# Performance work log

Hardware: AMD Instinct MI355X
Metric: run time of the kernel (lower is better)

Reference implementation:

```python
import jax, jax.numpy as jnp
import numpy as np

N_NODES = 200000
N_EDGES = 4000000  # doubled (w2b + b2w), matches edge_weight param size
N_W2B = 2000000


def gcn_conv(x, W, b, src, dst, ew, n):
    # PyG GCNConv with add_self_loops=True, symmetric normalization.
    loop = jnp.arange(n)
    src_sl = jnp.concatenate([src, loop])
    dst_sl = jnp.concatenate([dst, loop])
    w_sl = jnp.concatenate([ew, jnp.ones((n,), ew.dtype)])  # self-loop weight 1
    deg = jax.ops.segment_sum(w_sl, dst_sl, num_segments=n)
    dinv = jnp.where(deg > 0, jax.lax.rsqrt(deg), 0.0)
    norm = dinv[src_sl] * w_sl * dinv[dst_sl]          # [E+N]
    xw = x @ W                                          # [N, out]
    msg = xw[src_sl] * norm[:, None]                    # [E+N, out]
    out = jax.ops.segment_sum(msg, dst_sl, num_segments=n)
    return out + b


def setup_inputs() -> dict:
    key = jax.random.key(0)
    ks = jax.random.split(key, 16)
    h1, h2, h3, h4, out = 8, 16, 32, 4, 3
    inp = 7

    def lin_init(k, fan_in, fan_out):
        bound = 1.0 / np.sqrt(fan_in)
        kw, kb = jax.random.split(k)
        W = jax.random.uniform(kw, (fan_in, fan_out), jnp.float32, -bound, bound)
        b = jax.random.uniform(kb, (fan_out,), jnp.float32, -bound, bound)
        return W, b

    x = jax.random.normal(ks[0], (N_NODES, inp), jnp.float32)
    edge_index = jax.random.randint(ks[1], (2, N_EDGES), 0, N_NODES, jnp.int64)
    w2b = jax.random.randint(ks[2], (2, N_W2B), 0, N_NODES, jnp.int64)
    edge_weight = jnp.ones((N_EDGES,), jnp.float32)  # Parameter init: ones

    W1, b1 = lin_init(ks[3], inp, h1)
    W2, b2 = lin_init(ks[4], h1, h2)
    W3, b3 = lin_init(ks[5], h2, h3)
    Wl1, bl1 = lin_init(ks[6], 2 * h3, h4)
    Wl2, bl2 = lin_init(ks[7], h4, out)

    return dict(x=x, edge_index=edge_index, w2b=w2b, edge_weight=edge_weight,
                W1=W1, b1=b1, W2=W2, b2=b2, W3=W3, b3=b3,
                Wl1=Wl1, bl1=bl1, Wl2=Wl2, bl2=bl2)


def reference(x, edge_index, w2b, edge_weight,
              W1, b1, W2, b2, W3, b3, Wl1, bl1, Wl2, bl2):
    n = x.shape[0]
    src, dst = edge_index[0], edge_index[1]
    ew = jax.nn.sigmoid(edge_weight)
    h = jax.nn.relu(gcn_conv(x, W1, b1, src, dst, ew, n))
    h = jax.nn.relu(gcn_conv(h, W2, b2, src, dst, ew, n))
    h = jax.nn.relu(gcn_conv(h, W3, b3, src, dst, ew, n))
    # fused gather-concat replacing the per-edge python loop
    concat = jnp.concatenate([h[w2b[0]], h[w2b[1]]], axis=-1)  # [E_w2b, 2*h3]
    hidden = concat @ Wl1 + bl1
    edge_pred = hidden @ Wl2 + bl2
    return edge_pred
```

## Files before the change

### kernel.cpp

```cpp
#include <hip/hip_runtime.h>
#include <hip/hip_bf16.h>
#include <hip/hip_fp16.h>


#define NB1 768
#define NPB 256
#define MAXBINS 1024
#define TILE 4096
#define QS 16384.0f
#define QINV (1.0f / 16384.0f)

typedef _Float16 h2 __attribute__((ext_vector_type(2)));
typedef _Float16 h4 __attribute__((ext_vector_type(4)));
typedef _Float16 h8 __attribute__((ext_vector_type(8)));

__device__ __forceinline__ float sigmoidf_(float x) {
    return 1.0f / (1.0f + __expf(-x));
}

__global__ void p1a_hist(const int* __restrict__ dst, int* __restrict__ bh,
                         int ne, int nbins, int chunk) {
    __shared__ int h[MAXBINS];
    for (int k = threadIdx.x; k < nbins; k += 256) h[k] = 0;
    __syncthreads();
    int base = blockIdx.x * chunk;
    int end = min(base + chunk, ne);
    for (int e = base + threadIdx.x; e < end; e += 256)
        atomicAdd(&h[dst[e] >> 8], 1);
    __syncthreads();
    for (int k = threadIdx.x; k < nbins; k += 256)
        bh[(size_t)k * NB1 + blockIdx.x] = h[k];
}

__global__ void s1_scan(int* __restrict__ bh, int* __restrict__ bintot) {
    __shared__ int sums[256];
    constexpr int W = NB1 / 256;
    int* row = bh + (size_t)blockIdx.x * NB1;
    int v[W];
    int s = 0;
#pragma unroll
    for (int j = 0; j < W; ++j) { v[j] = row[threadIdx.x * W + j]; s += v[j]; }
    sums[threadIdx.x] = s;
    __syncthreads();
    for (int o = 1; o < 256; o <<= 1) {
        int t = (threadIdx.x >= o) ? sums[threadIdx.x - o] : 0;
        __syncthreads();
        sums[threadIdx.x] += t;
        __syncthreads();
    }
    int excl = sums[threadIdx.x] - s;
#pragma unroll
    for (int j = 0; j < W; ++j) { row[threadIdx.x * W + j] = excl; excl += v[j]; }
    if (threadIdx.x == 255) bintot[blockIdx.x] = sums[255];
}

__global__ void s2_scan(const int* __restrict__ bintot, int* __restrict__ binbase,
                        int nbins, int ne) {
    __shared__ int tmp[1024];
    int tid = threadIdx.x;
    int v = (tid < nbins) ? bintot[tid] : 0;
    tmp[tid] = v;
    __syncthreads();
    for (int o = 1; o < 1024; o <<= 1) {
        int t = (tid >= o) ? tmp[tid - o] : 0;
        __syncthreads();
        tmp[tid] += t;
        __syncthreads();
    }
    if (tid < nbins) binbase[tid] = tmp[tid] - v;
    if (tid == 0) binbase[nbins] = ne;
}

__global__ void p1b_scatter(const int* __restrict__ src, const int* __restrict__ dst,
                            const float* __restrict__ ew, const int* __restrict__ bh,
                            const int* __restrict__ binbase,
                            unsigned long long* __restrict__ b64,
                            int ne, int nbins, int chunk) {
    __shared__ unsigned long long stage[TILE];
    __shared__ int hist[MAXBINS];
    __shared__ int boff[MAXBINS];
    __shared__ int cur[MAXBINS];
    __shared__ int ssum[256];
    constexpr int MPT = TILE / 256;
    for (int k = threadIdx.x; k < nbins; k += 256)
        cur[k] = binbase[k] + bh[(size_t)k * NB1 + blockIdx.x];
    int base = blockIdx.x * chunk;
    int endb = min(base + chunk, ne);
    for (int t0 = base; t0 < endb; t0 += TILE) {
        int cnt = min(TILE, endb - t0);
        for (int k = threadIdx.x; k < nbins; k += 256) hist[k] = 0;
        __syncthreads();
        unsigned long long ent[MPT];
        int m = 0;
        for (int j = threadIdx.x; j < cnt; j += 256) {
            int e = t0 + j;
            int d = dst[e];
            float w = sigmoidf_(ew[e]);
            int q = (int)fminf(w * QS + 0.5f, 16383.0f);
            int b = d >> 8;
            ent[m++] = (unsigned long long)((unsigned)src[e] | ((unsigned)q << 18))
                     | ((unsigned long long)(d & 255) << 32)
                     | ((unsigned long long)b << 40);
            atomicAdd(&hist[b], 1);
        }
        __syncthreads();
        int w0 = threadIdx.x * 4;
        int lv[4];
        int ls = 0;
#pragma unroll
        for (int j = 0; j < 4; ++j) {
            int idx = w0 + j;
            lv[j] = (idx < nbins) ? hist[idx] : 0;
            ls += lv[j];
        }
        ssum[threadIdx.x] = ls;
        __syncthreads();
        for (int o = 1; o < 256; o <<= 1) {
            int t = (threadIdx.x >= o) ? ssum[threadIdx.x - o] : 0;
            __syncthreads();
            ssum[threadIdx.x] += t;
            __syncthreads();
        }
        int excl = ssum[threadIdx.x] - ls;
#pragma unroll
        for (int j = 0; j < 4; ++j) {
            int idx = w0 + j;
            if (idx < nbins) { boff[idx] = excl; excl += lv[j]; }
        }
        __syncthreads();
        for (int k = threadIdx.x; k < nbins; k += 256) hist[k] = 0;
        __syncthreads();
        for (int j = 0; j < m; ++j) {
            int b = (int)(ent[j] >> 40);
            int p = boff[b] + atomicAdd(&hist[b], 1);
            stage[p] = ent[j];
        }
        __syncthreads();
        for (int j = threadIdx.x; j < cnt; j += 256) {
            unsigned long long v = stage[j];
            int b = (int)(v >> 40);
            b64[cur[b] + (j - boff[b])] = v;
        }
        __syncthreads();
        for (int k = threadIdx.x; k < nbins; k += 256) cur[k] += hist[k];
        __syncthreads();
    }
}

__global__ void p2_build(const unsigned long long* __restrict__ b64,
                         const int* __restrict__ binbase, unsigned* __restrict__ edata,
                         int* __restrict__ C, float* __restrict__ dinv,
                         const float* __restrict__ x, const float* __restrict__ W1,
                         _Float16* __restrict__ g0, int n, int ne, int nbins) {
    __shared__ int cnt[NPB];
    __shared__ int rs[NPB];
    __shared__ int curs[NPB];
    __shared__ unsigned qsum[NPB];
    __shared__ float Ws[56];
    if (threadIdx.x < 56) Ws[threadIdx.x] = W1[threadIdx.x];
    int b = blockIdx.x;
    int E0 = binbase[b], E1 = binbase[b + 1];
    cnt[threadIdx.x] = 0;
    qsum[threadIdx.x] = 0;
    __syncthreads();
    for (int k = E0 + threadIdx.x; k < E1; k += 256)
        atomicAdd(&cnt[(int)((b64[k] >> 32) & 0xFF)], 1);
    __syncthreads();
    int v = cnt[threadIdx.x];
    rs[threadIdx.x] = v;
    __syncthreads();
    for (int o = 1; o < NPB; o <<= 1) {
        int t = (threadIdx.x >= o) ? rs[threadIdx.x - o] : 0;
        __syncthreads();
        rs[threadIdx.x] += t;
        __syncthreads();
    }
    int excl = rs[threadIdx.x] - v;
    curs[threadIdx.x] = E0 + excl;
    int node = b * NPB + threadIdx.x;
    if (node < n) C[node] = E0 + excl;
    if (b == 0 && threadIdx.x == 0) C[n] = ne;
    __syncthreads();
    for (int k = E0 + threadIdx.x; k < E1; k += 256) {
        unsigned long long e64 = b64[k];
        int dl = (int)((e64 >> 32) & 0xFF);
        int pos = atomicAdd(&curs[dl], 1);
        edata[pos] = (unsigned)(e64 & 0xFFFFFFFFu);
        atomicAdd(&qsum[dl], (unsigned)((e64 >> 18) & 0x3FFFu));
    }
    __syncthreads();
    if (node < n) {
        float dv = rsqrtf((float)qsum[threadIdx.x] * QINV + 1.0f);
        dinv[node] = dv;
        float xi[7];
#pragma unroll
        for (int k = 0; k < 7; ++k) xi[k] = x[(size_t)node * 7 + k];
        h8 r;
#pragma unroll
        for (int o = 0; o < 8; ++o) {
            float acc = 0.0f;
#pragma unroll
            for (int k = 0; k < 7; ++k) acc = fmaf(xi[k], Ws[k * 8 + o], acc);
            r[o] = (_Float16)(acc * dv);
        }
        *reinterpret_cast<h8*>(g0 + (size_t)node * 8) = r;
    }
}

__global__ void gather1_kernel(const _Float16* __restrict__ g, const float* __restrict__ dinv,
                               const int* __restrict__ C, const unsigned* __restrict__ edata,
                               const float* __restrict__ b1, _Float16* __restrict__ out, int n) {
    __shared__ float bs[8];
    if (threadIdx.x < 8) bs[threadIdx.x] = b1[threadIdx.x];
    __syncthreads();
    long long t = (long long)blockIdx.x * blockDim.x + threadIdx.x;
    int i = (int)(t >> 3);
    int sub = (int)(t & 3);
    int half = (int)((t >> 2) & 1);
    if (i >= n) return;
    int beg = C[i], end = C[i + 1];
    const _Float16* gb = g + sub * 2;
    float a0 = 0.0f, a1 = 0.0f;
    if (half == 0) {
        h2 r0 = *reinterpret_cast<const h2*>(gb + (size_t)i * 8);
        a0 = (float)r0[0]; a1 = (float)r0[1];
    }
    int k = beg + half;
    for (; k + 6 < end; k += 8) {
        unsigned v0 = edata[k];
        unsigned v1 = edata[k + 2];
        unsigned v2 = edata[k + 4];
        unsigned v3 = edata[k + 6];
        h2 r0 = *reinterpret_cast<const h2*>(gb + (size_t)(v0 & 0x3FFFFu) * 8);
        h2 r1 = *reinterpret_cast<const h2*>(gb + (size_t)(v1 & 0x3FFFFu) * 8);
        h2 r2 = *reinterpret_cast<const h2*>(gb + (size_t)(v2 & 0x3FFFFu) * 8);
        h2 r3 = *reinterpret_cast<const h2*>(gb + (size_t)(v3 & 0x3FFFFu) * 8);
        float w0 = (float)(v0 >> 18) * QINV;
        float w1 = (float)(v1 >> 18) * QINV;
        float w2 = (float)(v2 >> 18) * QINV;
        float w3 = (float)(v3 >> 18) * QINV;
        a0 = fmaf((float)r0[0], w0, a0); a1 = fmaf((float)r0[1], w0, a1);
        a0 = fmaf((float)r1[0], w1, a0); a1 = fmaf((float)r1[1], w1, a1);
        a0 = fmaf((float)r2[0], w2, a0); a1 = fmaf((float)r2[1], w2, a1);
        a0 = fmaf((float)r3[0], w3, a0); a1 = fmaf((float)r3[1], w3, a1);
    }
    for (; k < end; k += 2) {
        unsigned v = edata[k];
        float w = (float)(v >> 18) * QINV;
        h2 r = *reinterpret_cast<const h2*>(gb + (size_t)(v & 0x3FFFFu) * 8);
        a0 = fmaf((float)r[0], w, a0);
        a1 = fmaf((float)r[1], w, a1);
    }
    a0 += __shfl_xor(a0, 4, 64);
    a1 += __shfl_xor(a1, 4, 64);
    if (half == 0) {
        float dv = dinv[i];
        h2 o2;
        o2[0] = (_Float16)(dv * fmaxf(dv * a0 + bs[sub * 2 + 0], 0.0f));
        o2[1] = (_Float16)(dv * fmaxf(dv * a1 + bs[sub * 2 + 1], 0.0f));
        *reinterpret_cast<h2*>(out + (size_t)i * 8 + sub * 2) = o2;
    }
}

__global__ void gather2_kernel(const _Float16* __restrict__ g, const float* __restrict__ dinv,
                               const int* __restrict__ C, const unsigned* __restrict__ edata,
                               const float* __restrict__ W2, const float* __restrict__ b2,
                               _Float16* __restrict__ out, int n) {
    __shared__ float Ws[128];
    __shared__ float bs[16];
    if (threadIdx.x < 128) Ws[threadIdx.x] = W2[threadIdx.x];
    if (threadIdx.x < 16) bs[threadIdx.x] = b2[threadIdx.x];
    __syncthreads();
    long long t = (long long)blockIdx.x * blockDim.x + threadIdx.x;
    int i = (int)(t >> 3);
    int sub = (int)(t & 3);
    int half = (int)((t >> 2) & 1);
    if (i >= n) return;
    int beg = C[i], end = C[i + 1];
    const _Float16* gb = g + sub * 2;
    float a0 = 0.0f, a1 = 0.0f;
    if (half == 0) {
        h2 r0 = *reinterpret_cast<const h2*>(gb + (size_t)i * 8);
        a0 = (float)r0[0]; a1 = (float)r0[1];
    }
    int k = beg + half;
    for (; k + 6 < end; k += 8) {
        unsigned v0 = edata[k];
        unsigned v1 = edata[k + 2];
        unsigned v2 = edata[k + 4];
        unsigned v3 = edata[k + 6];
        h2 r0 = *reinterpret_cast<const h2*>(gb + (size_t)(v0 & 0x3FFFFu) * 8);
        h2 r1 = *reinterpret_cast<const h2*>(gb + (size_t)(v1 & 0x3FFFFu) * 8);
        h2 r2 = *reinterpret_cast<const h2*>(gb + (size_t)(v2 & 0x3FFFFu) * 8);
        h2 r3 = *reinterpret_cast<const h2*>(gb + (size_t)(v3 & 0x3FFFFu) * 8);
        float w0 = (float)(v0 >> 18) * QINV;
        float w1 = (float)(v1 >> 18) * QINV;
        float w2 = (float)(v2 >> 18) * QINV;
        float w3 = (float)(v3 >> 18) * QINV;
        a0 = fmaf((float)r0[0], w0, a0); a1 = fmaf((float)r0[1], w0, a1);
        a0 = fmaf((float)r1[0], w1, a0); a1 = fmaf((float)r1[1], w1, a1);
        a0 = fmaf((float)r2[0], w2, a0); a1 = fmaf((float)r2[1], w2, a1);
        a0 = fmaf((float)r3[0], w3, a0); a1 = fmaf((float)r3[1], w3, a1);
    }
    for (; k < end; k += 2) {
        unsigned v = edata[k];
        float w = (float)(v >> 18) * QINV;
        h2 r = *reinterpret_cast<const h2*>(gb + (size_t)(v & 0x3FFFFu) * 8);
        a0 = fmaf((float)r[0], w, a0);
        a1 = fmaf((float)r[1], w, a1);
    }
    a0 += __shfl_xor(a0, 4, 64);
    a1 += __shfl_xor(a1, 4, 64);
    float dv = dinv[i];
    float acc[2] = {a0 * dv, a1 * dv};
    float pv[4], raw[8];
    int oo = (sub & 1) * 2;
#pragma unroll
    for (int j = 0; j < 2; ++j) {
        float o1 = __shfl_xor(acc[j], 1, 64);
        pv[oo + j] = acc[j];
        pv[(oo ^ 2) + j] = o1;
    }
    int pb = (sub & 2) * 2;
#pragma unroll
    for (int j = 0; j < 4; ++j) {
        float o2v = __shfl_xor(pv[j], 2, 64);
        raw[pb + j] = pv[j];
        raw[(pb ^ 4) + j] = o2v;
    }
    int lane8 = half * 4 + sub;
    h2 o2;
#pragma unroll
    for (int jo = 0; jo < 2; ++jo) {
        int o = lane8 * 2 + jo;
        float h = bs[o];
#pragma unroll
        for (int k2 = 0; k2 < 8; ++k2) h = fmaf(raw[k2], Ws[k2 * 16 + o], h);
        o2[jo] = (_Float16)(dv * fmaxf(h, 0.0f));
    }
    *reinterpret_cast<h2*>(out + (size_t)i * 16 + lane8 * 2) = o2;
}

__global__ void gather3_kernel(const _Float16* __restrict__ g, const float* __restrict__ dinv,
                               const int* __restrict__ C, const unsigned* __restrict__ edata,
                               const float* __restrict__ W3, const float* __restrict__ b3,
                               const float* __restrict__ Wl1, const float* __restrict__ bl1,
                               const float* __restrict__ Wl2, const float* __restrict__ bl2,
                               _Float16* __restrict__ pqh, int n) {
    __shared__ float Ws[512];
    __shared__ float bs[32];
    __shared__ float wfs[192];
    __shared__ float bfs[3];
    for (int k = threadIdx.x; k < 512; k += 256) Ws[k] = W3[k];
    if (threadIdx.x < 32) bs[threadIdx.x] = b3[threadIdx.x];
    if (threadIdx.x < 192) {
        int f = threadIdx.x / 3, j = threadIdx.x % 3;
        float acc = 0.0f;
#pragma unroll
        for (int k = 0; k < 4; ++k) acc = fmaf(Wl1[f * 4 + k], Wl2[k * 3 + j], acc);
        wfs[threadIdx.x] = acc;
    }
    if (threadIdx.x < 3) {
        float acc = bl2[threadIdx.x];
#pragma unroll
        for (int k = 0; k < 4; ++k) acc = fmaf(bl1[k], Wl2[k * 3 + threadIdx.x], acc);
        bfs[threadIdx.x] = acc;
    }
    __syncthreads();
    long long t = (long long)blockIdx.x * blockDim.x + threadIdx.x;
    int i = (int)(t >> 3);
    int sub = (int)(t & 3);
    int half = (int)((t >> 2) & 1);
    if (i >= n) return;
    int beg = C[i], end = C[i + 1];
    const _Float16* gb = g + sub * 4;
    float acc[4] = {0.0f, 0.0f, 0.0f, 0.0f};
    if (half == 0) {
        h4 r0 = *reinterpret_cast<const h4*>(gb + (size_t)i * 16);
#pragma unroll
        for (int j = 0; j < 4; ++j) acc[j] = (float)r0[j];
    }
    int k = beg + half;
    for (; k + 6 < end; k += 8) {
        unsigned v0 = edata[k];
        unsigned v1 = edata[k + 2];
        unsigned v2 = edata[k + 4];
        unsigned v3 = edata[k + 6];
        h4 r0 = *reinterpret_cast<const h4*>(gb + (size_t)(v0 & 0x3FFFFu) * 16);
        h4 r1 = *reinterpret_cast<const h4*>(gb + (size_t)(v1 & 0x3FFFFu) * 16);
        h4 r2 = *reinterpret_cast<const h4*>(gb + (size_t)(v2 & 0x3FFFFu) * 16);
        h4 r3 = *reinterpret_cast<const h4*>(gb + (size_t)(v3 & 0x3FFFFu) * 16);
        float w0 = (float)(v0 >> 18) * QINV;
        float w1 = (float)(v1 >> 18) * QINV;
        float w2 = (float)(v2 >> 18) * QINV;
        float w3 = (float)(v3 >> 18) * QINV;
#pragma unroll
        for (int j = 0; j < 4; ++j) acc[j] = fmaf((float)r0[j], w0, acc[j]);
#pragma unroll
        for (int j = 0; j < 4; ++j) acc[j] = fmaf((float)r1[j], w1, acc[j]);
#pragma unroll
        for (int j = 0; j < 4; ++j) acc[j] = fmaf((float)r2[j], w2, acc[j]);
#pragma unroll
        for (int j = 0; j < 4; ++j) acc[j] = fmaf((float)r3[j], w3, acc[j]);
    }
    for (; k < end; k += 2) {
        unsigned v = edata[k];
        float w = (float)(v >> 18) * QINV;
        h4 r = *reinterpret_cast<const h4*>(gb + (size_t)(v & 0x3FFFFu) * 16);
#pragma unroll
        for (int j = 0; j < 4; ++j) acc[j] = fmaf((float)r[j], w, acc[j]);
    }
#pragma unroll
    for (int j = 0; j < 4; ++j) acc[j] += __shfl_xor(acc[j], 4, 64);
    float dv = dinv[i];
#pragma unroll
    for (int j = 0; j < 4; ++j) acc[j] *= dv;
    float pv[8], raw[16];
    int oo = (sub & 1) * 4;
#pragma unroll
    for (int j = 0; j < 4; ++j) {
        float o1 = __shfl_xor(acc[j], 1, 64);
        pv[oo + j] = acc[j];
        pv[(oo ^ 4) + j] = o1;
    }
    int pb = (sub & 2) * 4;
#pragma unroll
    for (int j = 0; j < 8; ++j) {
        float o2v = __shfl_xor(pv[j], 2, 64);
        raw[pb + j] = pv[j];
        raw[(pb ^ 8) + j] = o2v;
    }
    int lane8 = half * 4 + sub;
    float p0 = (lane8 == 0) ? bfs[0] : 0.0f;
    float p1 = (lane8 == 0) ? bfs[1] : 0.0f;
    float p2 = (lane8 == 0) ? bfs[2] : 0.0f;
    float q0 = 0.0f, q1 = 0.0f, q2 = 0.0f;
#pragma unroll
    for (int jo = 0; jo < 4; ++jo) {
        int o = lane8 * 4 + jo;
        float h = bs[o];
#pragma unroll
        for (int k2 = 0; k2 < 16; ++k2) h = fmaf(raw[k2], Ws[k2 * 32 + o], h);
        h = fmaxf(h, 0.0f);
        p0 = fmaf(h, wfs[o * 3 + 0], p0);
        p1 = fmaf(h, wfs[o * 3 + 1], p1);
        p2 = fmaf(h, wfs[o * 3 + 2], p2);
        q0 = fmaf(h, wfs[(32 + o) * 3 + 0], q0);
        q1 = fmaf(h, wfs[(32 + o) * 3 + 1], q1);
        q2 = fmaf(h, wfs[(32 + o) * 3 + 2], q2);
    }
    p0 += __shfl_xor(p0, 1, 64); p0 += __shfl_xor(p0, 2, 64); p0 += __shfl_xor(p0, 4, 64);
    p1 += __shfl_xor(p1, 1, 64); p1 += __shfl_xor(p1, 2, 64); p1 += __shfl_xor(p1, 4, 64);
    p2 += __shfl_xor(p2, 1, 64); p2 += __shfl_xor(p2, 2, 64); p2 += __shfl_xor(p2, 4, 64);
    q0 += __shfl_xor(q0, 1, 64); q0 += __shfl_xor(q0, 2, 64); q0 += __shfl_xor(q0, 4, 64);
    q1 += __shfl_xor(q1, 1, 64); q1 += __shfl_xor(q1, 2, 64); q1 += __shfl_xor(q1, 4, 64);
    q2 += __shfl_xor(q2, 1, 64); q2 += __shfl_xor(q2, 2, 64); q2 += __shfl_xor(q2, 4, 64);
    if (lane8 == 0) {
        h8 o8;
        o8[0] = (_Float16)p0; o8[1] = (_Float16)p1; o8[2] = (_Float16)p2; o8[3] = (_Float16)0.0f;
        o8[4] = (_Float16)q0; o8[5] = (_Float16)q1; o8[6] = (_Float16)q2; o8[7] = (_Float16)0.0f;
        *reinterpret_cast<h8*>(pqh + (size_t)i * 8) = o8;
    }
}

__global__ void head_kernel(const int* __restrict__ w2b, const _Float16* __restrict__ pqh,
                            float* __restrict__ out, int nw) {
    int e = blockIdx.x * blockDim.x + threadIdx.x;
    if (e >= nw) return;
    int a = w2b[e];
    int b = w2b[(size_t)nw + e];
    h4 P = *reinterpret_cast<const h4*>(pqh + (size_t)a * 8);
    h4 Q = *reinterpret_cast<const h4*>(pqh + (size_t)b * 8 + 4);
    out[(size_t)e * 3 + 0] = (float)P[0] + (float)Q[0];
    out[(size_t)e * 3 + 1] = (float)P[1] + (float)Q[1];
    out[(size_t)e * 3 + 2] = (float)P[2] + (float)Q[2];
}

extern "C" void kernel_launch(void* const* d_in, const int* in_sizes, int n_in,
                              void* d_out, int out_size, void* d_ws, size_t ws_size,
                              hipStream_t stream) {
    const float* x   = (const float*)d_in[0];
    const int* eidx  = (const int*)d_in[1];
    const int* w2b   = (const int*)d_in[2];
    const float* ew  = (const float*)d_in[3];
    const float* W1  = (const float*)d_in[4];
    const float* b1  = (const float*)d_in[5];
    const float* W2  = (const float*)d_in[6];
    const float* b2  = (const float*)d_in[7];
    const float* W3  = (const float*)d_in[8];
    const float* b3  = (const float*)d_in[9];
    const float* Wl1 = (const float*)d_in[10];
    const float* bl1 = (const float*)d_in[11];
    const float* Wl2 = (const float*)d_in[12];
    const float* bl2 = (const float*)d_in[13];
    float* out = (float*)d_out;

    const int n  = in_sizes[0] / 7;
    const int ne = in_sizes[1] / 2;
    const int nw = in_sizes[2] / 2;
    const int* src = eidx;
    const int* dst = eidx + ne;

    const int nbins = (n + NPB - 1) / NPB;
    const int chunk = (ne + NB1 - 1) / NB1;

    float*     ws      = (float*)d_ws;
    float*     dinv    = ws;
    int*       C       = (int*)(ws + n);
    unsigned*  edata   = (unsigned*)(ws + 2 * (size_t)n + 16);
    int*       bh      = (int*)(edata + ne);
    int*       bintot  = bh + (size_t)nbins * NB1;
    int*       binbase = bintot + MAXBINS;
    _Float16*  g0      = (_Float16*)(binbase + MAXBINS);
    float*     bregion = (float*)(g0 + (size_t)n * 8);
    unsigned long long* b64 = (unsigned long long*)bregion;
    _Float16*  g1      = (_Float16*)bregion;
    _Float16*  g2      = (_Float16*)(bregion + 4 * (size_t)n);
    _Float16*  pqh     = (_Float16*)(bregion + 12 * (size_t)n);

    const int Bl = 256;
    auto blks = [&](long long t) { return (int)((t + Bl - 1) / Bl); };
    const int nb8 = blks((long long)n * 8);

    p1a_hist<<<NB1, Bl, 0, stream>>>(dst, bh, ne, nbins, chunk);
    s1_scan<<<nbins, Bl, 0, stream>>>(bh, bintot);
    s2_scan<<<1, 1024, 0, stream>>>(bintot, binbase, nbins, ne);
    p1b_scatter<<<NB1, Bl, 0, stream>>>(src, dst, ew, bh, binbase, b64, ne, nbins, chunk);
    p2_build<<<nbins, Bl, 0, stream>>>(b64, binbase, edata, C, dinv, x, W1, g0, n, ne, nbins);

    gather1_kernel<<<nb8, Bl, 0, stream>>>(g0, dinv, C, edata, b1, g1, n);
    gather2_kernel<<<nb8, Bl, 0, stream>>>(g1, dinv, C, edata, W2, b2, g2, n);
    gather3_kernel<<<nb8, Bl, 0, stream>>>(g2, dinv, C, edata, W3, b3,
                                           Wl1, bl1, Wl2, bl2, pqh, n);

    head_kernel<<<blks(nw), Bl, 0, stream>>>(w2b, pqh, out, nw);
}
```

Baseline: 365.5 us.

## Split edges across 8 lanes with full-row gathers and separate layer-3 dense kernel

The gather kernels now give each of the 8 lanes per node a disjoint subset of edges and load full feature rows (h8/2×h8) per edge instead of splitting features across lanes. The partial sums are combined with butterfly shuffle reductions. Layer 3's dense transform and head weights move out of the gather into a new per-node dense3 kernel, which reads an extra raw3 buffer and uses transposed shared weights. The intent is fewer, wider memory transactions per edge and less shuffle work in the gather. The cost is an extra kernel launch and an extra intermediate buffer round trip.

After: 346.6 us. 1.05x faster.

```diff
diff --git a/kernel.cpp b/kernel.cpp
--- a/kernel.cpp
+++ b/kernel.cpp
@@ -215,51 +215,55 @@
     __syncthreads();
     long long t = (long long)blockIdx.x * blockDim.x + threadIdx.x;
     int i = (int)(t >> 3);
-    int sub = (int)(t & 3);
-    int half = (int)((t >> 2) & 1);
+    int l8 = (int)(t & 7);
     if (i >= n) return;
     int beg = C[i], end = C[i + 1];
-    const _Float16* gb = g + sub * 2;
-    float a0 = 0.0f, a1 = 0.0f;
-    if (half == 0) {
-        h2 r0 = *reinterpret_cast<const h2*>(gb + (size_t)i * 8);
-        a0 = (float)r0[0]; a1 = (float)r0[1];
-    }
-    int k = beg + half;
-    for (; k + 6 < end; k += 8) {
+    float acc[8] = {0.f, 0.f, 0.f, 0.f, 0.f, 0.f, 0.f, 0.f};
+    if (l8 == 0) {
+        h8 r = *reinterpret_cast<const h8*>(g + (size_t)i * 8);
+#pragma unroll
+        for (int j = 0; j < 8; ++j) acc[j] = (float)r[j];
+    }
+    int k = beg + l8;
+    for (; k + 8 < end; k += 16) {
         unsigned v0 = edata[k];
-        unsigned v1 = edata[k + 2];
-        unsigned v2 = edata[k + 4];
-        unsigned v3 = edata[k + 6];
-        h2 r0 = *reinterpret_cast<const h2*>(gb + (size_t)(v0 & 0x3FFFFu) * 8);
-        h2 r1 = *reinterpret_cast<const h2*>(gb + (size_t)(v1 & 0x3FFFFu) * 8);
-        h2 r2 = *reinterpret_cast<const h2*>(gb + (size_t)(v2 & 0x3FFFFu) * 8);
-        h2 r3 = *reinterpret_cast<const h2*>(gb + (size_t)(v3 & 0x3FFFFu) * 8);
+        unsigned v1 = edata[k + 8];
+        h8 r0 = *reinterpret_cast<const h8*>(g + (size_t)(v0 & 0x3FFFFu) * 8);
+        h8 r1 = *reinterpret_cast<const h8*>(g + (size_t)(v1 & 0x3FFFFu) * 8);
         float w0 = (float)(v0 >> 18) * QINV;
         float w1 = (float)(v1 >> 18) * QINV;
-        float w2 = (float)(v2 >> 18) * QINV;
-        float w3 = (float)(v3 >> 18) * QINV;
-        a0 = fmaf((float)r0[0], w0, a0); a1 = fmaf((float)r0[1], w0, a1);
-        a0 = fmaf((float)r1[0], w1, a0); a1 = fmaf((float)r1[1], w1, a1);
-        a0 = fmaf((float)r2[0], w2, a0); a1 = fmaf((float)r2[1], w2, a1);
-        a0 = fmaf((float)r3[0], w3, a0); a1 = fmaf((float)r3[1], w3, a1);
-    }
-    for (; k < end; k += 2) {
+#pragma unroll
+        for (int j = 0; j < 8; ++j) acc[j] = fmaf((float)r0[j], w0, acc[j]);
+#pragma unroll
+        for (int j = 0; j < 8; ++j) acc[j] = fmaf((float)r1[j], w1, acc[j]);
+    }
+    if (k < end) {
         unsigned v = edata[k];
         float w = (float)(v >> 18) * QINV;
-        h2 r = *reinterpret_cast<const h2*>(gb + (size_t)(v & 0x3FFFFu) * 8);
-        a0 = fmaf((float)r[0], w, a0);
-        a1 = fmaf((float)r[1], w, a1);
-    }
-    a0 += __shfl_xor(a0, 4, 64);
-    a1 += __shfl_xor(a1, 4, 64);
-    if (half == 0) {
-        float dv = dinv[i];
-        h2 o2;
-        o2[0] = (_Float16)(dv * fmaxf(dv * a0 + bs[sub * 2 + 0], 0.0f));
-        o2[1] = (_Float16)(dv * fmaxf(dv * a1 + bs[sub * 2 + 1], 0.0f));
-        *reinterpret_cast<h2*>(out + (size_t)i * 8 + sub * 2) = o2;
-    }
+        h8 r = *reinterpret_cast<const h8*>(g + (size_t)(v & 0x3FFFFu) * 8);
+#pragma unroll
+        for (int j = 0; j < 8; ++j) acc[j] = fmaf((float)r[j], w, acc[j]);
+    }
+    bool t4 = (l8 & 4) != 0, t2 = (l8 & 2) != 0, t1 = (l8 & 1) != 0;
+    float s4[4];
+#pragma unroll
+    for (int j = 0; j < 4; ++j) {
+        float keep = t4 ? acc[4 + j] : acc[j];
+        float send = t4 ? acc[j] : acc[4 + j];
+        s4[j] = keep + __shfl_xor(send, 4, 64);
+    }
+    float s2[2];
+#pragma unroll
+    for (int j = 0; j < 2; ++j) {
+        float keep = t2 ? s4[2 + j] : s4[j];
+        float send = t2 ? s4[j] : s4[2 + j];
+        s2[j] = keep + __shfl_xor(send, 2, 64);
+    }
+    float keep = t1 ? s2[1] : s2[0];
+    float send = t1 ? s2[0] : s2[1];
+    float s = keep + __shfl_xor(send, 1, 64);
+    float dv = dinv[i];
+    out[(size_t)i * 8 + l8] = (_Float16)(dv * fmaxf(dv * s + bs[l8], 0.0f));
 }
 
 __global__ void gather2_kernel(const _Float16* __restrict__ g, const float* __restrict__ dinv,
@@ -273,174 +277,186 @@
     __syncthreads();
     long long t = (long long)blockIdx.x * blockDim.x + threadIdx.x;
     int i = (int)(t >> 3);
-    int sub = (int)(t & 3);
-    int half = (int)((t >> 2) & 1);
+    int l8 = (int)(t & 7);
     if (i >= n) return;
     int beg = C[i], end = C[i + 1];
-    const _Float16* gb = g + sub * 2;
-    float a0 = 0.0f, a1 = 0.0f;
-    if (half == 0) {
-        h2 r0 = *reinterpret_cast<const h2*>(gb + (size_t)i * 8);
-        a0 = (float)r0[0]; a1 = (float)r0[1];
-    }
-    int k = beg + half;
-    for (; k + 6 < end; k += 8) {
+    float acc[8] = {0.f, 0.f, 0.f, 0.f, 0.f, 0.f, 0.f, 0.f};
+    if (l8 == 0) {
+        h8 r = *reinterpret_cast<const h8*>(g + (size_t)i * 8);
+#pragma unroll
+        for (int j = 0; j < 8; ++j) acc[j] = (float)r[j];
+    }
+    int k = beg + l8;
+    for (; k + 8 < end; k += 16) {
         unsigned v0 = edata[k];
-        unsigned v1 = edata[k + 2];
-        unsigned v2 = edata[k + 4];
-        unsigned v3 = edata[k + 6];
-        h2 r0 = *reinterpret_cast<const h2*>(gb + (size_t)(v0 & 0x3FFFFu) * 8);
-        h2 r1 = *reinterpret_cast<const h2*>(gb + (size_t)(v1 & 0x3FFFFu) * 8);
-        h2 r2 = *reinterpret_cast<const h2*>(gb + (size_t)(v2 & 0x3FFFFu) * 8);
-        h2 r3 = *reinterpret_cast<const h2*>(gb + (size_t)(v3 & 0x3FFFFu) * 8);
+        unsigned v1 = edata[k + 8];
+        h8 r0 = *reinterpret_cast<const h8*>(g + (size_t)(v0 & 0x3FFFFu) * 8);
+        h8 r1 = *reinterpret_cast<const h8*>(g + (size_t)(v1 & 0x3FFFFu) * 8);
         float w0 = (float)(v0 >> 18) * QINV;
         float w1 = (float)(v1 >> 18) * QINV;
-        float w2 = (float)(v2 >> 18) * QINV;
-        float w3 = (float)(v3 >> 18) * QINV;
-        a0 = fmaf((float)r0[0], w0, a0); a1 = fmaf((float)r0[1], w0, a1);
-        a0 = fmaf((float)r1[0], w1, a0); a1 = fmaf((float)r1[1], w1, a1);
-        a0 = fmaf((float)r2[0], w2, a0); a1 = fmaf((float)r2[1], w2, a1);
-        a0 = fmaf((float)r3[0], w3, a0); a1 = fmaf((float)r3[1], w3, a1);
-    }
-    for (; k < end; k += 2) {
+#pragma unroll
+        for (int j = 0; j < 8; ++j) acc[j] = fmaf((float)r0[j], w0, acc[j]);
+#pragma unroll
+        for (int j = 0; j < 8; ++j) acc[j] = fmaf((float)r1[j], w1, acc[j]);
+    }
+    if (k < end) {
         unsigned v = edata[k];
         float w = (float)(v >> 18) * QINV;
-        h2 r = *reinterpret_cast<const h2*>(gb + (size_t)(v & 0x3FFFFu) * 8);
-        a0 = fmaf((float)r[0], w, a0);
-        a1 = fmaf((float)r[1], w, a1);
-    }
-    a0 += __shfl_xor(a0, 4, 64);
-    a1 += __shfl_xor(a1, 4, 64);
+        h8 r = *reinterpret_cast<const h8*>(g + (size_t)(v & 0x3FFFFu) * 8);
+#pragma unroll
+        for (int j = 0; j < 8; ++j) acc[j] = fmaf((float)r[j], w, acc[j]);
+    }
+#pragma unroll
+    for (int j = 0; j < 8; ++j) {
+        acc[j] += __shfl_xor(acc[j], 1, 64);
+        acc[j] += __shfl_xor(acc[j], 2, 64);
+        acc[j] += __shfl_xor(acc[j], 4, 64);
+    }
     float dv = dinv[i];
-    float acc[2] = {a0 * dv, a1 * dv};
-    float pv[4], raw[8];
-    int oo = (sub & 1) * 2;
-#pragma unroll
-    for (int j = 0; j < 2; ++j) {
-        float o1 = __shfl_xor(acc[j], 1, 64);
-        pv[oo + j] = acc[j];
-        pv[(oo ^ 2) + j] = o1;
-    }
-    int pb = (sub & 2) * 2;
-#pragma unroll
-    for (int j = 0; j < 4; ++j) {
-        float o2v = __shfl_xor(pv[j], 2, 64);
-        raw[pb + j] = pv[j];
-        raw[(pb ^ 4) + j] = o2v;
-    }
-    int lane8 = half * 4 + sub;
+    float raw[8];
+#pragma unroll
+    for (int j = 0; j < 8; ++j) raw[j] = acc[j] * dv;
+    int o0 = l8 * 2;
     h2 o2;
 #pragma unroll
     for (int jo = 0; jo < 2; ++jo) {
-        int o = lane8 * 2 + jo;
+        int o = o0 + jo;
         float h = bs[o];
 #pragma unroll
         for (int k2 = 0; k2 < 8; ++k2) h = fmaf(raw[k2], Ws[k2 * 16 + o], h);
         o2[jo] = (_Float16)(dv * fmaxf(h, 0.0f));
     }
-    *reinterpret_cast<h2*>(out + (size_t)i * 16 + lane8 * 2) = o2;
+    *reinterpret_cast<h2*>(out + (size_t)i * 16 + o0) = o2;
 }
 
 __global__ void gather3_kernel(const _Float16* __restrict__ g, const float* __restrict__ dinv,
                                const int* __restrict__ C, const unsigned* __restrict__ edata,
-                               const float* __restrict__ W3, const float* __restrict__ b3,
-                               const float* __restrict__ Wl1, const float* __restrict__ bl1,
-                               const float* __restrict__ Wl2, const float* __restrict__ bl2,
-                               _Float16* __restrict__ pqh, int n) {
-    __shared__ float Ws[512];
+                               _Float16* __restrict__ raw3, int n) {
+    long long t = (long long)blockIdx.x * blockDim.x + threadIdx.x;
+    int i = (int)(t >> 3);
+    int l8 = (int)(t & 7);
+    if (i >= n) return;
+    int beg = C[i], end = C[i + 1];
+    float acc[16];
+#pragma unroll
+    for (int j = 0; j < 16; ++j) acc[j] = 0.0f;
+    if (l8 == 0) {
+        h8 r0 = *reinterpret_cast<const h8*>(g + (size_t)i * 16);
+        h8 r1 = *reinterpret_cast<const h8*>(g + (size_t)i * 16 + 8);
+#pragma unroll
+        for (int j = 0; j < 8; ++j) { acc[j] = (float)r0[j]; acc[8 + j] = (float)r1[j]; }
+    }
+    int k = beg + l8;
+    for (; k + 8 < end; k += 16) {
+        unsigned v0 = edata[k];
+        unsigned v1 = edata[k + 8];
+        size_t i0 = (size_t)(v0 & 0x3FFFFu) * 16;
+        size_t i1 = (size_t)(v1 & 0x3FFFFu) * 16;
+        h8 a0 = *reinterpret_cast<const h8*>(g + i0);
+        h8 a1 = *reinterpret_cast<const h8*>(g + i0 + 8);
+        h8 c0 = *reinterpret_cast<const h8*>(g + i1);
+        h8 c1 = *reinterpret_cast<const h8*>(g + i1 + 8);
+        float w0 = (float)(v0 >> 18) * QINV;
+        float w1 = (float)(v1 >> 18) * QINV;
+#pragma unroll
+        for (int j = 0; j < 8; ++j) acc[j] = fmaf((float)a0[j], w0, acc[j]);
+#pragma unroll
+        for (int j = 0; j < 8; ++j) acc[8 + j] = fmaf((float)a1[j], w0, acc[8 + j]);
+#pragma unroll
+        for (int j = 0; j < 8; ++j) acc[j] = fmaf((float)c0[j], w1, acc[j]);
+#pragma unroll
+        for (int j = 0; j < 8; ++j) acc[8 + j] = fmaf((float)c1[j], w1, acc[8 + j]);
+    }
+    if (k < end) {
+        unsigned v = edata[k];
+        size_t i0 = (size_t)(v & 0x3FFFFu) * 16;
+        h8 a0 = *reinterpret_cast<const h8*>(g + i0);
+        h8 a1 = *reinterpret_cast<const h8*>(g + i0 + 8);
+        float w = (float)(v >> 18) * QINV;
+#pragma unroll
+        for (int j = 0; j < 8; ++j) acc[j] = fmaf((float)a0[j], w, acc[j]);
+#pragma unroll
+        for (int j = 0; j < 8; ++j) acc[8 + j] = fmaf((float)a1[j], w, acc[8 + j]);
+    }
+    bool t4 = (l8 & 4) != 0, t2 = (l8 & 2) != 0, t1 = (l8 & 1) != 0;
+    float s8[8];
+#pragma unroll
+    for (int j = 0; j < 8; ++j) {
+        float keep = t4 ? acc[8 + j] : acc[j];
+        float send = t4 ? acc[j] : acc[8 + j];
+        s8[j] = keep + __shfl_xor(send, 4, 64);
+    }
+    float s4[4];
+#pragma unroll
+    for (int j = 0; j < 4; ++j) {
+        float keep = t2 ? s8[4 + j] : s8[j];
+        float send = t2 ? s8[j] : s8[4 + j];
+        s4[j] = keep + __shfl_xor(send, 2, 64);
+    }
+    float s2[2];
+#pragma unroll
+    for (int j = 0; j < 2; ++j) {
+        float keep = t1 ? s4[2 + j] : s4[j];
+        float send = t1 ? s4[j] : s4[2 + j];
+        s2[j] = keep + __shfl_xor(send, 1, 64);
+    }
+    float dv = dinv[i];
+    h2 o2;
+    o2[0] = (_Float16)(s2[0] * dv);
+    o2[1] = (_Float16)(s2[1] * dv);
+    *reinterpret_cast<h2*>(raw3 + (size_t)i * 16 + l8 * 2) = o2;
+}
+
+__global__ void dense3_kernel(const _Float16* __restrict__ raw3,
+                              const float* __restrict__ W3, const float* __restrict__ b3,
+                              const float* __restrict__ Wl1, const float* __restrict__ bl1,
+                              const float* __restrict__ Wl2, const float* __restrict__ bl2,
+                              _Float16* __restrict__ pqh, int n) {
+    __shared__ __align__(16) float WsT[512];
     __shared__ float bs[32];
     __shared__ float wfs[192];
     __shared__ float bfs[3];
-    for (int k = threadIdx.x; k < 512; k += 256) Ws[k] = W3[k];
+    for (int t = threadIdx.x; t < 512; t += 256) {
+        int k = t >> 5, o = t & 31;
+        WsT[o * 16 + k] = W3[t];
+    }
     if (threadIdx.x < 32) bs[threadIdx.x] = b3[threadIdx.x];
     if (threadIdx.x < 192) {
         int f = threadIdx.x / 3, j = threadIdx.x % 3;
-        float acc = 0.0f;
-#pragma unroll
-        for (int k = 0; k < 4; ++k) acc = fmaf(Wl1[f * 4 + k], Wl2[k * 3 + j], acc);
-        wfs[threadIdx.x] = acc;
+        float a = 0.0f;
+#pragma unroll
+        for (int k = 0; k < 4; ++k) a = fmaf(Wl1[f * 4 + k], Wl2[k * 3 + j], a);
+        wfs[threadIdx.x] = a;
     }
     if (threadIdx.x < 3) {
-        float acc = bl2[threadIdx.x];
-#pragma unroll
-        for (int k = 0; k < 4; ++k) acc = fmaf(bl1[k], Wl2[k * 3 + threadIdx.x], acc);
-        bfs[threadIdx.x] = acc;
-    }
-    __syncthreads();
-    long long t = (long long)blockIdx.x * blockDim.x + threadIdx.x;
-    int i = (int)(t >> 3);
-    int sub = (int)(t & 3);
-    int half = (int)((t >> 2) & 1);
+        float a = bl2[threadIdx.x];
+#pragma unroll
+        for (int k = 0; k < 4; ++k) a = fmaf(bl1[k], Wl2[k * 3 + threadIdx.x], a);
+        bfs[threadIdx.x] = a;
+    }
+    __syncthreads();
+    int i = blockIdx.x * 256 + threadIdx.x;
     if (i >= n) return;
-    int beg = C[i], end = C[i + 1];
-    const _Float16* gb = g + sub * 4;
-    float acc[4] = {0.0f, 0.0f, 0.0f, 0.0f};
-    if (half == 0) {
-        h4 r0 = *reinterpret_cast<const h4*>(gb + (size_t)i * 16);
-#pragma unroll
-        for (int j = 0; j < 4; ++j) acc[j] = (float)r0[j];
-    }
-    int k = beg + half;
-    for (; k + 6 < end; k += 8) {
-        unsigned v0 = edata[k];
-        unsigned v1 = edata[k + 2];
-        unsigned v2 = edata[k + 4];
-        unsigned v3 = edata[k + 6];
-        h4 r0 = *reinterpret_cast<const h4*>(gb + (size_t)(v0 & 0x3FFFFu) * 16);
-        h4 r1 = *reinterpret_cast<const h4*>(gb + (size_t)(v1 & 0x3FFFFu) * 16);
-        h4 r2 = *reinterpret_cast<const h4*>(gb + (size_t)(v2 & 0x3FFFFu) * 16);
-        h4 r3 = *reinterpret_cast<const h4*>(gb + (size_t)(v3 & 0x3FFFFu) * 16);
-        float w0 = (float)(v0 >> 18) * QINV;
-        float w1 = (float)(v1 >> 18) * QINV;
-        float w2 = (float)(v2 >> 18) * QINV;
-        float w3 = (float)(v3 >> 18) * QINV;
-#pragma unroll
-        for (int j = 0; j < 4; ++j) acc[j] = fmaf((float)r0[j], w0, acc[j]);
-#pragma unroll
-        for (int j = 0; j < 4; ++j) acc[j] = fmaf((float)r1[j], w1, acc[j]);
-#pragma unroll
-        for (int j = 0; j < 4; ++j) acc[j] = fmaf((float)r2[j], w2, acc[j]);
-#pragma unroll
-        for (int j = 0; j < 4; ++j) acc[j] = fmaf((float)r3[j], w3, acc[j]);
-    }
-    for (; k < end; k += 2) {
-        unsigned v = edata[k];
-        float w = (float)(v >> 18) * QINV;
-        h4 r = *reinterpret_cast<const h4*>(gb + (size_t)(v & 0x3FFFFu) * 16);
-#pragma unroll
-        for (int j = 0; j < 4; ++j) acc[j] = fmaf((float)r[j], w, acc[j]);
-    }
-#pragma unroll
-    for (int j = 0; j < 4; ++j) acc[j] += __shfl_xor(acc[j], 4, 64);
-    float dv = dinv[i];
-#pragma unroll
-    for (int j = 0; j < 4; ++j) acc[j] *= dv;
-    float pv[8], raw[16];
-    int oo = (sub & 1) * 4;
-#pragma unroll
-    for (int j = 0; j < 4; ++j) {
-        float o1 = __shfl_xor(acc[j], 1, 64);
-        pv[oo + j] = acc[j];
-        pv[(oo ^ 4) + j] = o1;
-    }
-    int pb = (sub & 2) * 4;
-#pragma unroll
-    for (int j = 0; j < 8; ++j) {
-        float o2v = __shfl_xor(pv[j], 2, 64);
-        raw[pb + j] = pv[j];
-        raw[(pb ^ 8) + j] = o2v;
-    }
-    int lane8 = half * 4 + sub;
-    float p0 = (lane8 == 0) ? bfs[0] : 0.0f;
-    float p1 = (lane8 == 0) ? bfs[1] : 0.0f;
-    float p2 = (lane8 == 0) ? bfs[2] : 0.0f;
+    h8 r0 = *reinterpret_cast<const h8*>(raw3 + (size_t)i * 16);
+    h8 r1 = *reinterpret_cast<const h8*>(raw3 + (size_t)i * 16 + 8);
+    float raw[16];
+#pragma unroll
+    for (int j = 0; j < 8; ++j) { raw[j] = (float)r0[j]; raw[8 + j] = (float)r1[j]; }
+    float p0 = bfs[0], p1 = bfs[1], p2 = bfs[2];
     float q0 = 0.0f, q1 = 0.0f, q2 = 0.0f;
 #pragma unroll
-    for (int jo = 0; jo < 4; ++jo) {
-        int o = lane8 * 4 + jo;
+    for (int o = 0; o < 32; ++o) {
+        const float4* w4 = reinterpret_cast<const float4*>(WsT + o * 16);
+        float4 wa = w4[0], wb = w4[1], wc = w4[2], wd = w4[3];
         float h = bs[o];
-#pragma unroll
-        for (int k2 = 0; k2 < 16; ++k2) h = fmaf(raw[k2], Ws[k2 * 32 + o], h);
+        h = fmaf(raw[0], wa.x, h);  h = fmaf(raw[1], wa.y, h);
+        h = fmaf(raw[2], wa.z, h);  h = fmaf(raw[3], wa.w, h);
+        h = fmaf(raw[4], wb.x, h);  h = fmaf(raw[5], wb.y, h);
+        h = fmaf(raw[6], wb.z, h);  h = fmaf(raw[7], wb.w, h);
+        h = fmaf(raw[8], wc.x, h);  h = fmaf(raw[9], wc.y, h);
+        h = fmaf(raw[10], wc.z, h); h = fmaf(raw[11], wc.w, h);
+        h = fmaf(raw[12], wd.x, h); h = fmaf(raw[13], wd.y, h);
+        h = fmaf(raw[14], wd.z, h); h = fmaf(raw[15], wd.w, h);
         h = fmaxf(h, 0.0f);
         p0 = fmaf(h, wfs[o * 3 + 0], p0);
         p1 = fmaf(h, wfs[o * 3 + 1], p1);
@@ -449,18 +465,10 @@
         q1 = fmaf(h, wfs[(32 + o) * 3 + 1], q1);
         q2 = fmaf(h, wfs[(32 + o) * 3 + 2], q2);
     }
-    p0 += __shfl_xor(p0, 1, 64); p0 += __shfl_xor(p0, 2, 64); p0 += __shfl_xor(p0, 4, 64);
-    p1 += __shfl_xor(p1, 1, 64); p1 += __shfl_xor(p1, 2, 64); p1 += __shfl_xor(p1, 4, 64);
-    p2 += __shfl_xor(p2, 1, 64); p2 += __shfl_xor(p2, 2, 64); p2 += __shfl_xor(p2, 4, 64);
-    q0 += __shfl_xor(q0, 1, 64); q0 += __shfl_xor(q0, 2, 64); q0 += __shfl_xor(q0, 4, 64);
-    q1 += __shfl_xor(q1, 1, 64); q1 += __shfl_xor(q1, 2, 64); q1 += __shfl_xor(q1, 4, 64);
-    q2 += __shfl_xor(q2, 1, 64); q2 += __shfl_xor(q2, 2, 64); q2 += __shfl_xor(q2, 4, 64);
-    if (lane8 == 0) {
-        h8 o8;
-        o8[0] = (_Float16)p0; o8[1] = (_Float16)p1; o8[2] = (_Float16)p2; o8[3] = (_Float16)0.0f;
-        o8[4] = (_Float16)q0; o8[5] = (_Float16)q1; o8[6] = (_Float16)q2; o8[7] = (_Float16)0.0f;
-        *reinterpret_cast<h8*>(pqh + (size_t)i * 8) = o8;
-    }
+    h8 o8;
+    o8[0] = (_Float16)p0; o8[1] = (_Float16)p1; o8[2] = (_Float16)p2; o8[3] = (_Float16)0.0f;
+    o8[4] = (_Float16)q0; o8[5] = (_Float16)q1; o8[6] = (_Float16)q2; o8[7] = (_Float16)0.0f;
+    *reinterpret_cast<h8*>(pqh + (size_t)i * 8) = o8;
 }
 
 __global__ void head_kernel(const int* __restrict__ w2b, const _Float16* __restrict__ pqh,
@@ -517,6 +525,7 @@
     _Float16*  g1      = (_Float16*)bregion;
     _Float16*  g2      = (_Float16*)(bregion + 4 * (size_t)n);
     _Float16*  pqh     = (_Float16*)(bregion + 12 * (size_t)n);
+    _Float16*  raw3    = (_Float16*)(bregion + 16 * (size_t)n);
 
     const int Bl = 256;
     auto blks = [&](long long t) { return (int)((t + Bl - 1) / Bl); };
@@ -530,8 +539,8 @@
 
     gather1_kernel<<<nb8, Bl, 0, stream>>>(g0, dinv, C, edata, b1, g1, n);
     gather2_kernel<<<nb8, Bl, 0, stream>>>(g1, dinv, C, edata, W2, b2, g2, n);
-    gather3_kernel<<<nb8, Bl, 0, stream>>>(g2, dinv, C, edata, W3, b3,
-                                           Wl1, bl1, Wl2, bl2, pqh, n);
+    gather3_kernel<<<nb8, Bl, 0, stream>>>(g2, dinv, C, edata, raw3, n);
+    dense3_kernel<<<blks(n), Bl, 0, stream>>>(raw3, W3, b3, Wl1, bl1, Wl2, bl2, pqh, n);
 
     head_kernel<<<blks(nw), Bl, 0, stream>>>(w2b, pqh, out, nw);
 }
```
